# Optimization experiments

Hardware: AMD Instinct MI355X
Metric: run time of the kernel (lower is better)

Reference implementation:

```python
import jax, jax.numpy as jnp
import numpy as np

EPS = 1e-07


def setup_inputs() -> dict:
    key = jax.random.key(0)
    k1, k2, k3 = jax.random.split(key, 3)
    B, C, H, W, K = 4, 64, 512, 512, 19
    x = jax.random.normal(k1, (B, C, H, W), dtype=jnp.float32)
    gt = jax.random.randint(k2, (B, H, W), 0, K, dtype=jnp.int32)
    aug_rand_info = jax.random.uniform(k3, (B, K, K), dtype=jnp.float32)
    return {"x": x, "gt": gt, "aug_rand_info": aug_rand_info}


def reference(x, gt, aug_rand_info):
    # x: [B,C,H,W], gt: [B,H,W] int labels in [0,K), aug_rand_info: [B,K,K]
    B, C, H, W = x.shape
    K = aug_rand_info.shape[1]
    HW = H * W
    # global segment id = b*K + class
    seg = (jnp.arange(B, dtype=jnp.int32)[:, None] * K + gt.reshape(B, HW)).reshape(-1)
    xf = x.reshape(B, C, HW).transpose(0, 2, 1).reshape(B * HW, C)  # [B*HW, C]
    # per-(image,class) sums and counts (segment reduce)
    sums = jax.ops.segment_sum(xf, seg, num_segments=B * K).reshape(B, K, C)
    cnt = jax.ops.segment_sum(jnp.ones((B * HW,), x.dtype), seg, num_segments=B * K).reshape(B, K, 1)
    valid = cnt > 0
    cnt_safe = jnp.where(valid, cnt, jnp.ones_like(cnt))
    mean = sums / cnt_safe                                     # [B,K,C]
    mean_px = mean.reshape(B * K, C)[seg]                      # gather per pixel
    var = jax.ops.segment_sum((xf - mean_px) ** 2, seg, num_segments=B * K).reshape(B, K, C) / cnt_safe
    std = jnp.sqrt(var) + EPS                                  # [B,K,C]
    # Dirichlet-style mixing weights over classes present in each image
    validf = valid.astype(x.dtype).reshape(B, 1, K)            # [B,1,K]
    w = aug_rand_info * validf                                 # zero out absent source classes
    w = w / jnp.clip(w.sum(-1, keepdims=True), EPS)            # renormalize -> simplex
    mix_mean = jnp.einsum('bck,bkd->bcd', w, mean)             # [B,K,C] style mean per target class
    mix_std = jnp.einsum('bck,bkd->bcd', w, std)
    # fused gather + per-class normalize + style scatter (class masks are disjoint)
    idx = gt.reshape(B, HW)[:, :, None]                        # [B,HW,1]
    take = lambda t: jnp.take_along_axis(t, idx, axis=1)       # [B,HW,C]
    m, s = take(mean), take(std)
    mm, ms = take(mix_mean), take(mix_std)
    xn = (xf.reshape(B, HW, C) - m) / s * ms + mm
    x_style = xn.transpose(0, 2, 1).reshape(B, C, H, W)
    return x_style
```

## Files before the change

kernel.cpp:

```cpp
#include <hip/hip_runtime.h>

#define EPSF 1e-7f

constexpr int Bn = 4, Cn = 64, Kn = 19;
constexpr int HWn = 512 * 512;

constexpr int SCH   = 64;
constexpr int SPIX  = HWn / SCH;
constexpr int SBLK  = 1024;
constexpr int HPIX  = 2048;
constexpr int TSTR  = 2052;
constexpr int PARTSZ = 2464;

typedef float f32x16_t __attribute__((ext_vector_type(16)));
typedef float f32x4_t  __attribute__((ext_vector_type(4)));
typedef short bf16x8_t __attribute__((ext_vector_type(8)));

#define PKBF(lo, hi) ((__builtin_bit_cast(unsigned, (hi)) & 0xFFFF0000u) | \
                      (__builtin_bit_cast(unsigned, (lo)) >> 16))

__global__ __launch_bounds__(SBLK, 4) void k_stats(
    const float* __restrict__ x, const int* __restrict__ gt,
    float* __restrict__ part)
{
    __shared__ unsigned short tile[32 * TSTR];
    __shared__ int   lab[SPIX];
    __shared__ float credL[32];

    const int tid  = threadIdx.x;
    const int lane = tid & 63;
    const int w    = tid >> 6;
    const int g    = lane >> 5;
    const int col  = lane & 31;

    const int b    = blockIdx.x >> 6;
    const int pix0 = (blockIdx.x & 63) * SPIX;
    const float* xb  = x  + (size_t)b * Cn * HWn + pix0;
    const int*   gtb = gt + (size_t)b * HWn + pix0;

    {
        const int4 v = *reinterpret_cast<const int4*>(gtb + tid * 4);
        int4 cl;
        cl.x = min(max(v.x, 0), Kn - 1); cl.y = min(max(v.y, 0), Kn - 1);
        cl.z = min(max(v.z, 0), Kn - 1); cl.w = min(max(v.w, 0), Kn - 1);
        *reinterpret_cast<int4*>(&lab[tid * 4]) = cl;
    }

    f32x16_t dS0 = (f32x16_t)0.f, dQ0 = (f32x16_t)0.f;
    f32x16_t dS1 = (f32x16_t)0.f, dQ1 = (f32x16_t)0.f;
    int cnt = 0;

#define STAGE_(G, H) { \
    _Pragma("unroll") \
    for (int cc = 0; cc < 2; ++cc) { \
        const float* src = xb + (size_t)((G)*32 + w*2 + cc) * HWn + (H) * HPIX; \
        unsigned short* dst = &tile[(w*2 + cc) * TSTR]; \
        _Pragma("unroll") \
        for (int i = 0; i < 8; ++i) { \
            const float4 v = *reinterpret_cast<const float4*>(src + i*256 + lane*4); \
            uint2 pk; pk.x = PKBF(v.x, v.y); pk.y = PKBF(v.z, v.w); \
            *reinterpret_cast<uint2*>(&dst[i*256 + lane*4]) = pk; \
        } \
    } }

#define COMPUTE_(H, DS, DQ, CNTON) { \
    _Pragma("unroll 1") \
    for (int s = 0; s < 8; ++s) { \
        const int pg = w*128 + s*16 + 8*g; \
        const unsigned short* trow = &tile[col * TSTR + pg]; \
        const uint2 bA = *reinterpret_cast<const uint2*>(trow); \
        const uint2 bB = *reinterpret_cast<const uint2*>(trow + 4); \
        int4 bv; bv.x = (int)bA.x; bv.y = (int)bA.y; bv.z = (int)bB.x; bv.w = (int)bB.y; \
        int4 bq; \
        { \
            const float f0 = __builtin_bit_cast(float, bA.x << 16); \
            const float f1 = __builtin_bit_cast(float, bA.x & 0xFFFF0000u); \
            const float f2 = __builtin_bit_cast(float, bA.y << 16); \
            const float f3 = __builtin_bit_cast(float, bA.y & 0xFFFF0000u); \
            const float f4 = __builtin_bit_cast(float, bB.x << 16); \
            const float f5 = __builtin_bit_cast(float, bB.x & 0xFFFF0000u); \
            const float f6 = __builtin_bit_cast(float, bB.y << 16); \
            const float f7 = __builtin_bit_cast(float, bB.y & 0xFFFF0000u); \
            bq.x = PKBF(f0*f0, f1*f1); bq.y = PKBF(f2*f2, f3*f3); \
            bq.z = PKBF(f4*f4, f5*f5); bq.w = PKBF(f6*f6, f7*f7); \
        } \
        const int4 L0 = *reinterpret_cast<const int4*>(&lab[(H)*HPIX + pg]); \
        const int4 L1 = *reinterpret_cast<const int4*>(&lab[(H)*HPIX + pg + 4]); \
        const bool e0=(L0.x==col), e1=(L0.y==col), e2=(L0.z==col), e3=(L0.w==col); \
        const bool e4=(L1.x==col), e5=(L1.y==col), e6=(L1.z==col), e7=(L1.w==col); \
        int4 av; \
        av.x = (e0?0x3F80u:0u) | (e1?0x3F800000u:0u); \
        av.y = (e2?0x3F80u:0u) | (e3?0x3F800000u:0u); \
        av.z = (e4?0x3F80u:0u) | (e5?0x3F800000u:0u); \
        av.w = (e6?0x3F80u:0u) | (e7?0x3F800000u:0u); \
        if (CNTON) cnt += (int)e0+(int)e1+(int)e2+(int)e3+(int)e4+(int)e5+(int)e6+(int)e7; \
        DS = __builtin_amdgcn_mfma_f32_32x32x16_bf16( \
                 __builtin_bit_cast(bf16x8_t, av), __builtin_bit_cast(bf16x8_t, bv), DS, 0, 0, 0); \
        DQ = __builtin_amdgcn_mfma_f32_32x32x16_bf16( \
                 __builtin_bit_cast(bf16x8_t, av), __builtin_bit_cast(bf16x8_t, bq), DQ, 0, 0, 0); \
    } }

    STAGE_(0, 0)
    __syncthreads();
    COMPUTE_(0, dS0, dQ0, true)
    __syncthreads();
    STAGE_(1, 0)
    __syncthreads();
    COMPUTE_(0, dS1, dQ1, false)
    __syncthreads();
    STAGE_(0, 1)
    __syncthreads();
    COMPUTE_(1, dS0, dQ0, true)
    __syncthreads();
    STAGE_(1, 1)
    __syncthreads();
    COMPUTE_(1, dS1, dQ1, false)

    const int cnt2 = cnt + __shfl(cnt, col + 32, 64);

    __syncthreads();
    float* redf = reinterpret_cast<float*>(tile);
    #pragma unroll 1
    for (int ww = 0; ww < 16; ++ww) {
        if (w == ww) {
            #pragma unroll
            for (int r = 0; r < 16; ++r) {
                const int krow = (r & 3) + 8 * (r >> 2) + 4 * g;
                if (krow < Kn) {
                    float* bse = &redf[krow * 128];
                    if (ww == 0) {
                        bse[col]           = dS0[r];  bse[64 + col]      = dQ0[r];
                        bse[32 + col]      = dS1[r];  bse[96 + col]      = dQ1[r];
                    } else {
                        bse[col]          += dS0[r];  bse[64 + col]     += dQ0[r];
                        bse[32 + col]     += dS1[r];  bse[96 + col]     += dQ1[r];
                    }
                }
            }
            if (lane < Kn) {
                if (ww == 0) credL[lane]  = (float)cnt2;
                else         credL[lane] += (float)cnt2;
            }
        }
        __syncthreads();
    }

    float* pb = part + (size_t)blockIdx.x * PARTSZ;
    for (int i = tid; i < 2 * Cn * Kn; i += SBLK) {
        const int stat = i / (Cn * Kn);
        const int rr   = i - stat * (Cn * Kn);
        const int c = rr / Kn, k = rr - c * Kn;
        pb[i] = redf[k * 128 + stat * 64 + c];
    }
    if (tid < Kn) pb[2 * Cn * Kn + tid] = credL[tid];
}

__global__ __launch_bounds__(1024) void k_tables(
    const float* __restrict__ part, const float* __restrict__ aug,
    float* __restrict__ tabAB)
{
    __shared__ float mean_s[Kn * Cn];
    __shared__ float std_s [Kn * Cn];
    __shared__ float wrow  [Kn * Kn];
    __shared__ float wsum  [Kn];
    __shared__ float validf[Kn], cntf[Kn];

    const int b = blockIdx.x, tid = threadIdx.x;
    const float* pbase = part + (size_t)b * SCH * PARTSZ;

    if (tid < Kn) {
        float s = 0.f;
        for (int blk = 0; blk < SCH; ++blk)
            s += pbase[(size_t)blk * PARTSZ + 2 * Cn * Kn + tid];
        validf[tid] = (s > 0.f) ? 1.f : 0.f;
        cntf[tid]   = (s > 0.f) ? s : 1.f;
    }
    __syncthreads();

    for (int i = tid; i < Cn * Kn; i += 1024) {
        float s = 0.f, q = 0.f;
        for (int blk = 0; blk < SCH; ++blk) {
            s += pbase[(size_t)blk * PARTSZ + i];
            q += pbase[(size_t)blk * PARTSZ + Cn * Kn + i];
        }
        const int c = i / Kn, k = i - c * Kn;
        const float cs  = cntf[k];
        const float m   = s / cs;
        const float var = fmaxf(q / cs - m * m, 0.f);
        mean_s[k * Cn + c] = m;
        std_s [k * Cn + c] = sqrtf(var) + EPSF;
    }
    for (int i = tid; i < Kn * Kn; i += 1024) {
        const int t = i / Kn, k = i - t * Kn;
        wrow[i] = aug[((size_t)b * Kn + t) * Kn + k] * validf[k];
    }
    __syncthreads();
    if (tid < Kn) {
        float s = 0.f;
        for (int k = 0; k < Kn; ++k) s += wrow[tid * Kn + k];
        wsum[tid] = fmaxf(s, EPSF);
    }
    __syncthreads();
    for (int i = tid; i < Kn * Cn; i += 1024) {
        const int t = i >> 6, c = i & 63;
        const float inv = 1.f / wsum[t];
        float mm = 0.f, ms = 0.f;
        for (int k = 0; k < Kn; ++k) {
            const float wk = wrow[t * Kn + k] * inv;
            mm += wk * mean_s[k * Cn + c];
            ms += wk * std_s [k * Cn + c];
        }
        const float A  = ms / std_s[t * Cn + c];
        const float Bv = mm - mean_s[t * Cn + c] * A;
        const size_t o = ((size_t)b * Cn * Kn + c * Kn + t) * 2;
        tabAB[o + 0] = A;
        tabAB[o + 1] = Bv;
    }
}

constexpr int ABLK = 1024;
constexpr int ACH  = 64;
constexpr int APIX = HWn / ACH;

__global__ __launch_bounds__(ABLK, 4) void k_apply(
    const float* __restrict__ x, const int* __restrict__ gt,
    const float* __restrict__ tabAB, float* __restrict__ out)
{
    __shared__ float ABs[Cn * Kn * 2];
    const int tid   = threadIdx.x;
    const int b     = blockIdx.x >> 6;
    const int chunk = blockIdx.x & 63;

    for (int i = tid; i < Cn * Kn * 2; i += ABLK)
        ABs[i] = tabAB[(size_t)b * Cn * Kn * 2 + i];
    __syncthreads();

    const int p0 = chunk * APIX + tid * 4;
    const int4 L = *reinterpret_cast<const int4*>(gt + (size_t)b * HWn + p0);
    const int l0 = min(max(L.x, 0), Kn - 1);
    const int l1 = min(max(L.y, 0), Kn - 1);
    const int l2 = min(max(L.z, 0), Kn - 1);
    const int l3 = min(max(L.w, 0), Kn - 1);

    const float* xp = x   + (size_t)b * Cn * HWn + p0;
    float*       op = out + (size_t)b * Cn * HWn + p0;

    #pragma unroll 4
    for (int c = 0; c < Cn; ++c) {
        const float4 v = *reinterpret_cast<const float4*>(xp + (size_t)c * HWn);
        const int co = c * Kn;
        const float2 ab0 = *reinterpret_cast<const float2*>(&ABs[(co + l0) * 2]);
        const float2 ab1 = *reinterpret_cast<const float2*>(&ABs[(co + l1) * 2]);
        const float2 ab2 = *reinterpret_cast<const float2*>(&ABs[(co + l2) * 2]);
        const float2 ab3 = *reinterpret_cast<const float2*>(&ABs[(co + l3) * 2]);
        float4 o;
        o.x = v.x * ab0.x + ab0.y;
        o.y = v.y * ab1.x + ab1.y;
        o.z = v.z * ab2.x + ab2.y;
        o.w = v.w * ab3.x + ab3.y;
        __builtin_nontemporal_store(__builtin_bit_cast(f32x4_t, o),
                                    reinterpret_cast<f32x4_t*>(op + (size_t)c * HWn));
    }
}

extern "C" void kernel_launch(void* const* d_in, const int* in_sizes, int n_in,
                              void* d_out, int out_size, void* d_ws, size_t ws_size,
                              hipStream_t stream) {
    const float* x   = (const float*)d_in[0];
    const int*   gt  = (const int*)d_in[1];
    const float* aug = (const float*)d_in[2];
    float* out = (float*)d_out;

    float* part  = (float*)d_ws;
    float* tabAB = part + (size_t)Bn * SCH * PARTSZ;

    k_stats <<<dim3(Bn * SCH), dim3(SBLK), 0, stream>>>(x, gt, part);
    k_tables<<<dim3(Bn),       dim3(1024), 0, stream>>>(part, aug, tabAB);
    k_apply <<<dim3(Bn * ACH), dim3(ABLK), 0, stream>>>(x, gt, tabAB, out);
}
```

Baseline: 170.5 us.

## Pack sum and square columns into one MFMA per step in stats kernel

Restructures the stats kernel so each 32-wide MFMA B operand carries 16 channels of raw values in lanes 0-15 and their squares in lanes 16-31. One MFMA per step then produces both sums and sums of squares, where the old code issued two MFMAs (S and Q) per step. Staging now covers 16 channels over all pixels per round across four rounds, with a matching remap of the reduction indices. The aim is to halve MFMA count and LDS B-reads. The cost is a divergent branch for squaring within a wave, an extra sync, and more stage/compute rounds.

After: 178.2 us. +4.5%, slower.

```diff
diff --git a/kernel.cpp b/kernel.cpp
--- a/kernel.cpp
+++ b/kernel.cpp
@@ -8,8 +8,7 @@
 constexpr int SCH   = 64;
 constexpr int SPIX  = HWn / SCH;
 constexpr int SBLK  = 1024;
-constexpr int HPIX  = 2048;
-constexpr int TSTR  = 2052;
+constexpr int TSTR  = 4104;
 constexpr int PARTSZ = 2464;
 
 typedef float f32x16_t __attribute__((ext_vector_type(16)));
@@ -23,7 +22,7 @@
     const float* __restrict__ x, const int* __restrict__ gt,
     float* __restrict__ part)
 {
-    __shared__ unsigned short tile[32 * TSTR];
+    __shared__ unsigned short tile[16 * TSTR];
     __shared__ int   lab[SPIX];
     __shared__ float credL[32];
 
@@ -32,6 +31,7 @@
     const int w    = tid >> 6;
     const int g    = lane >> 5;
     const int col  = lane & 31;
+    const int ch16 = col & 15;
 
     const int b    = blockIdx.x >> 6;
     const int pix0 = (blockIdx.x & 63) * SPIX;
@@ -46,97 +46,88 @@
         *reinterpret_cast<int4*>(&lab[tid * 4]) = cl;
     }
 
-    f32x16_t dS0 = (f32x16_t)0.f, dQ0 = (f32x16_t)0.f;
-    f32x16_t dS1 = (f32x16_t)0.f, dQ1 = (f32x16_t)0.f;
+    f32x16_t dR0 = (f32x16_t)0.f, dR1 = (f32x16_t)0.f;
+    f32x16_t dR2 = (f32x16_t)0.f, dR3 = (f32x16_t)0.f;
     int cnt = 0;
 
-#define STAGE_(G, H) { \
+#define STAGE_(R) { \
+    const float* src = xb + (size_t)((R) * 16 + w) * HWn; \
+    unsigned short* dst = &tile[w * TSTR]; \
     _Pragma("unroll") \
-    for (int cc = 0; cc < 2; ++cc) { \
-        const float* src = xb + (size_t)((G)*32 + w*2 + cc) * HWn + (H) * HPIX; \
-        unsigned short* dst = &tile[(w*2 + cc) * TSTR]; \
-        _Pragma("unroll") \
-        for (int i = 0; i < 8; ++i) { \
-            const float4 v = *reinterpret_cast<const float4*>(src + i*256 + lane*4); \
-            uint2 pk; pk.x = PKBF(v.x, v.y); pk.y = PKBF(v.z, v.w); \
-            *reinterpret_cast<uint2*>(&dst[i*256 + lane*4]) = pk; \
+    for (int i = 0; i < 16; ++i) { \
+        const float4 v = *reinterpret_cast<const float4*>(src + i * 256 + lane * 4); \
+        uint2 pk; pk.x = PKBF(v.x, v.y); pk.y = PKBF(v.z, v.w); \
+        *reinterpret_cast<uint2*>(&dst[i * 256 + lane * 4]) = pk; \
+    } }
+
+#define COMPUTE_(R, D, CNTON) { \
+    _Pragma("unroll 1") \
+    for (int s = 0; s < 16; ++s) { \
+        const int pg = w * 256 + s * 16 + 8 * g; \
+        uint4 bw = *reinterpret_cast<const uint4*>(&tile[ch16 * TSTR + pg]); \
+        if (col >= 16) { \
+            const float f0 = __builtin_bit_cast(float, bw.x << 16); \
+            const float f1 = __builtin_bit_cast(float, bw.x & 0xFFFF0000u); \
+            const float f2 = __builtin_bit_cast(float, bw.y << 16); \
+            const float f3 = __builtin_bit_cast(float, bw.y & 0xFFFF0000u); \
+            const float f4 = __builtin_bit_cast(float, bw.z << 16); \
+            const float f5 = __builtin_bit_cast(float, bw.z & 0xFFFF0000u); \
+            const float f6 = __builtin_bit_cast(float, bw.w << 16); \
+            const float f7 = __builtin_bit_cast(float, bw.w & 0xFFFF0000u); \
+            bw.x = PKBF(f0 * f0, f1 * f1); bw.y = PKBF(f2 * f2, f3 * f3); \
+            bw.z = PKBF(f4 * f4, f5 * f5); bw.w = PKBF(f6 * f6, f7 * f7); \
         } \
+        const int4 L0 = *reinterpret_cast<const int4*>(&lab[pg]); \
+        const int4 L1 = *reinterpret_cast<const int4*>(&lab[pg + 4]); \
+        const bool e0 = (L0.x == col), e1 = (L0.y == col); \
+        const bool e2 = (L0.z == col), e3 = (L0.w == col); \
+        const bool e4 = (L1.x == col), e5 = (L1.y == col); \
+        const bool e6 = (L1.z == col), e7 = (L1.w == col); \
+        int4 av; \
+        av.x = (e0 ? 0x3F80u : 0u) | (e1 ? 0x3F800000u : 0u); \
+        av.y = (e2 ? 0x3F80u : 0u) | (e3 ? 0x3F800000u : 0u); \
+        av.z = (e4 ? 0x3F80u : 0u) | (e5 ? 0x3F800000u : 0u); \
+        av.w = (e6 ? 0x3F80u : 0u) | (e7 ? 0x3F800000u : 0u); \
+        if (CNTON) cnt += (int)e0 + (int)e1 + (int)e2 + (int)e3 \
+                        + (int)e4 + (int)e5 + (int)e6 + (int)e7; \
+        D = __builtin_amdgcn_mfma_f32_32x32x16_bf16( \
+                __builtin_bit_cast(bf16x8_t, av), \
+                __builtin_bit_cast(bf16x8_t, bw), D, 0, 0, 0); \
     } }
 
-#define COMPUTE_(H, DS, DQ, CNTON) { \
-    _Pragma("unroll 1") \
-    for (int s = 0; s < 8; ++s) { \
-        const int pg = w*128 + s*16 + 8*g; \
-        const unsigned short* trow = &tile[col * TSTR + pg]; \
-        const uint2 bA = *reinterpret_cast<const uint2*>(trow); \
-        const uint2 bB = *reinterpret_cast<const uint2*>(trow + 4); \
-        int4 bv; bv.x = (int)bA.x; bv.y = (int)bA.y; bv.z = (int)bB.x; bv.w = (int)bB.y; \
-        int4 bq; \
-        { \
-            const float f0 = __builtin_bit_cast(float, bA.x << 16); \
-            const float f1 = __builtin_bit_cast(float, bA.x & 0xFFFF0000u); \
-            const float f2 = __builtin_bit_cast(float, bA.y << 16); \
-            const float f3 = __builtin_bit_cast(float, bA.y & 0xFFFF0000u); \
-            const float f4 = __builtin_bit_cast(float, bB.x << 16); \
-            const float f5 = __builtin_bit_cast(float, bB.x & 0xFFFF0000u); \
-            const float f6 = __builtin_bit_cast(float, bB.y << 16); \
-            const float f7 = __builtin_bit_cast(float, bB.y & 0xFFFF0000u); \
-            bq.x = PKBF(f0*f0, f1*f1); bq.y = PKBF(f2*f2, f3*f3); \
-            bq.z = PKBF(f4*f4, f5*f5); bq.w = PKBF(f6*f6, f7*f7); \
-        } \
-        const int4 L0 = *reinterpret_cast<const int4*>(&lab[(H)*HPIX + pg]); \
-        const int4 L1 = *reinterpret_cast<const int4*>(&lab[(H)*HPIX + pg + 4]); \
-        const bool e0=(L0.x==col), e1=(L0.y==col), e2=(L0.z==col), e3=(L0.w==col); \
-        const bool e4=(L1.x==col), e5=(L1.y==col), e6=(L1.z==col), e7=(L1.w==col); \
-        int4 av; \
-        av.x = (e0?0x3F80u:0u) | (e1?0x3F800000u:0u); \
-        av.y = (e2?0x3F80u:0u) | (e3?0x3F800000u:0u); \
-        av.z = (e4?0x3F80u:0u) | (e5?0x3F800000u:0u); \
-        av.w = (e6?0x3F80u:0u) | (e7?0x3F800000u:0u); \
-        if (CNTON) cnt += (int)e0+(int)e1+(int)e2+(int)e3+(int)e4+(int)e5+(int)e6+(int)e7; \
-        DS = __builtin_amdgcn_mfma_f32_32x32x16_bf16( \
-                 __builtin_bit_cast(bf16x8_t, av), __builtin_bit_cast(bf16x8_t, bv), DS, 0, 0, 0); \
-        DQ = __builtin_amdgcn_mfma_f32_32x32x16_bf16( \
-                 __builtin_bit_cast(bf16x8_t, av), __builtin_bit_cast(bf16x8_t, bq), DQ, 0, 0, 0); \
+    __syncthreads();
+    STAGE_(0)
+    __syncthreads();
+    COMPUTE_(0, dR0, true)
+    __syncthreads();
+    STAGE_(1)
+    __syncthreads();
+    COMPUTE_(1, dR1, false)
+    __syncthreads();
+    STAGE_(2)
+    __syncthreads();
+    COMPUTE_(2, dR2, false)
+    __syncthreads();
+    STAGE_(3)
+    __syncthreads();
+    COMPUTE_(3, dR3, false)
+
+    const int cnt2 = cnt + __shfl(cnt, col + 32, 64);
+
+    __syncthreads();
+    float* redf = reinterpret_cast<float*>(tile);
+    const int statO = (col >> 4) * 64;
+#define RED_(R, D, OP) { \
+    _Pragma("unroll") \
+    for (int r = 0; r < 16; ++r) { \
+        const int krow = (r & 3) + 8 * (r >> 2) + 4 * g; \
+        if (krow < Kn) redf[krow * 128 + statO + (R) * 16 + ch16] OP D[r]; \
     } }
-
-    STAGE_(0, 0)
-    __syncthreads();
-    COMPUTE_(0, dS0, dQ0, true)
-    __syncthreads();
-    STAGE_(1, 0)
-    __syncthreads();
-    COMPUTE_(0, dS1, dQ1, false)
-    __syncthreads();
-    STAGE_(0, 1)
-    __syncthreads();
-    COMPUTE_(1, dS0, dQ0, true)
-    __syncthreads();
-    STAGE_(1, 1)
-    __syncthreads();
-    COMPUTE_(1, dS1, dQ1, false)
-
-    const int cnt2 = cnt + __shfl(cnt, col + 32, 64);
-
-    __syncthreads();
-    float* redf = reinterpret_cast<float*>(tile);
     #pragma unroll 1
     for (int ww = 0; ww < 16; ++ww) {
         if (w == ww) {
-            #pragma unroll
-            for (int r = 0; r < 16; ++r) {
-                const int krow = (r & 3) + 8 * (r >> 2) + 4 * g;
-                if (krow < Kn) {
-                    float* bse = &redf[krow * 128];
-                    if (ww == 0) {
-                        bse[col]           = dS0[r];  bse[64 + col]      = dQ0[r];
-                        bse[32 + col]      = dS1[r];  bse[96 + col]      = dQ1[r];
-                    } else {
-                        bse[col]          += dS0[r];  bse[64 + col]     += dQ0[r];
-                        bse[32 + col]     += dS1[r];  bse[96 + col]     += dQ1[r];
-                    }
-                }
-            }
+            if (ww == 0) { RED_(0, dR0, =)  RED_(1, dR1, =)  RED_(2, dR2, =)  RED_(3, dR3, =) }
+            else         { RED_(0, dR0, +=) RED_(1, dR1, +=) RED_(2, dR2, +=) RED_(3, dR3, +=) }
             if (lane < Kn) {
                 if (ww == 0) credL[lane]  = (float)cnt2;
                 else         credL[lane] += (float)cnt2;
```
